# Kernel optimization log

Hardware: AMD Instinct MI355X
Metric: run time of the kernel (lower is better)

Reference implementation:

```python
import jax, jax.numpy as jnp
import numpy as np

IN_FEATURES = 4096
OUT_FEATURES = 4096
GROUP_SIZE = 128
TOKENS = 8192


def setup_inputs() -> dict:
    key = jax.random.key(0)
    k1, k2, k3 = jax.random.split(key, 3)
    x = jax.random.normal(k1, (TOKENS, IN_FEATURES), dtype=jnp.float32)
    weight_packed = jax.random.randint(k2, (OUT_FEATURES, IN_FEATURES // 2), 0, 256, dtype=jnp.int32)
    num_groups = IN_FEATURES // GROUP_SIZE
    weight_scales = jax.random.uniform(k3, (OUT_FEATURES, num_groups), dtype=jnp.float32) * 0.02
    return {"x": x, "weight_packed": weight_packed, "weight_scales": weight_scales, "group_size": GROUP_SIZE}


def _dequantize_int4(packed, scales, group_size):
    # packed: [N, K//2] int (uint8 values); scales: [N, G]
    out_features = packed.shape[0]
    in_features = packed.shape[1] * 2
    low = (packed & 15) - 8   # even columns
    high = ((packed >> 4) & 15) - 8  # odd columns
    # interleave low/high along last axis -> [N, K]
    unpacked = jnp.stack([low, high], axis=-1).reshape(out_features, in_features)
    num_groups = in_features // group_size
    w = unpacked.reshape(out_features, num_groups, group_size).astype(scales.dtype)
    w = w * scales[:, :, None]  # per-group scale
    return w.reshape(out_features, in_features)


def reference(x, weight_packed, weight_scales, group_size):
    W = _dequantize_int4(weight_packed, weight_scales, group_size)  # [N, K]
    # nn.functional.linear: x @ W.T (bias=False)
    return jnp.einsum('tk,nk->tn', x, W)
```

## Files before the change

### kernel.cpp

```cpp
#include <hip/hip_runtime.h>
#include <hip/hip_bf16.h>
#include <cstdint>
#include <cstddef>

#define TOKENS 8192
#define IN_F   4096
#define OUT_F  4096

typedef __bf16 bf16;
typedef bf16  bf16x8 __attribute__((ext_vector_type(8)));
typedef float f32x4  __attribute__((ext_vector_type(4)));

__global__ void prep_kernel(const float* __restrict__ xin, bf16* __restrict__ xout,
                            const int* __restrict__ wp, const float* __restrict__ sc,
                            bf16* __restrict__ wout) {
    if (blockIdx.x < 16384) {
        size_t i = ((size_t)blockIdx.x * 256 + threadIdx.x) * 8;
        const float4* p = (const float4*)(xin + i);
        float4 a = p[0], b = p[1];
        bf16x8 r;
        r[0] = (bf16)a.x; r[1] = (bf16)a.y; r[2] = (bf16)a.z; r[3] = (bf16)a.w;
        r[4] = (bf16)b.x; r[5] = (bf16)b.y; r[6] = (bf16)b.z; r[7] = (bf16)b.w;
        *(bf16x8*)(xout + i) = r;
    } else {
        int t  = (blockIdx.x - 16384) * 256 + threadIdx.x;
        int j0 = t << 2;
        int n  = j0 >> 11;
        int g  = (j0 & 2047) >> 6;
        float s = sc[(n << 5) + g];
        int4 p = *(const int4*)(wp + j0);
        bf16x8 r;
        r[0] = (bf16)((float)((p.x & 15) - 8) * s);
        r[1] = (bf16)((float)(((p.x >> 4) & 15) - 8) * s);
        r[2] = (bf16)((float)((p.y & 15) - 8) * s);
        r[3] = (bf16)((float)(((p.y >> 4) & 15) - 8) * s);
        r[4] = (bf16)((float)((p.z & 15) - 8) * s);
        r[5] = (bf16)((float)(((p.z >> 4) & 15) - 8) * s);
        r[6] = (bf16)((float)((p.w & 15) - 8) * s);
        r[7] = (bf16)((float)(((p.w >> 4) & 15) - 8) * s);
        *(bf16x8*)(wout + ((size_t)j0 << 1)) = r;
    }
}

__global__ void gemm_kernel(const bf16* __restrict__ A, const bf16* __restrict__ B,
                            float* __restrict__ C) {
    __shared__ char smem[32768] __attribute__((aligned(128)));

    const int tid  = threadIdx.x;
    const int lane = tid & 63;
    const int w    = tid >> 6;
    const int mt   = blockIdx.x >> 5;
    const int nt   = blockIdx.x & 31;

    const char* ga[4]; const char* gb[4]; int ldsoff[4];
#pragma unroll
    for (int t = 0; t < 4; ++t) {
        int c   = (w * 4 + t) * 64 + lane;
        int row = c >> 3;
        int g   = (c & 7) ^ (row & 7);
        ga[t] = (const char*)A + (size_t)(mt * 128 + row) * (IN_F * 2) + g * 16;
        gb[t] = (const char*)B + (size_t)(nt * 128 + row) * (IN_F * 2) + g * 16;
        ldsoff[t] = (w * 4 + t) * 1024;
    }

    const int m_lane = lane & 15;
    const int quad   = lane >> 4;
    const int sw     = m_lane & 7;
    const int m0     = (w >> 1) * 64;
    const int n0     = (w & 1) * 64;

    f32x4 acc[4][4];
#pragma unroll
    for (int i = 0; i < 4; ++i)
#pragma unroll
        for (int j = 0; j < 4; ++j) acc[i][j] = (f32x4)0.0f;

    const bf16x8* pA = (const bf16x8*)smem;
    const bf16x8* pB = (const bf16x8*)(smem + 16384);

    for (int kt = 0; kt < IN_F / 64; ++kt) {
#pragma unroll
        for (int t = 0; t < 4; ++t) {
            __builtin_amdgcn_global_load_lds(
                (const __attribute__((address_space(1))) void*)(ga[t] + kt * 128),
                (__attribute__((address_space(3))) void*)(smem + ldsoff[t]), 16, 0, 0);
            __builtin_amdgcn_global_load_lds(
                (const __attribute__((address_space(1))) void*)(gb[t] + kt * 128),
                (__attribute__((address_space(3))) void*)(smem + 16384 + ldsoff[t]), 16, 0, 0);
        }
        __syncthreads();

#pragma unroll
        for (int h = 0; h < 2; ++h) {
            const int slot = (h * 4 + quad) ^ sw;
            bf16x8 af[4], bfr[4];
#pragma unroll
            for (int i = 0; i < 4; ++i)
                af[i] = pA[(m0 + i * 16 + m_lane) * 8 + slot];
#pragma unroll
            for (int j = 0; j < 4; ++j)
                bfr[j] = pB[(n0 + j * 16 + m_lane) * 8 + slot];
#pragma unroll
            for (int i = 0; i < 4; ++i)
#pragma unroll
                for (int j = 0; j < 4; ++j)
                    acc[i][j] = __builtin_amdgcn_mfma_f32_16x16x32_bf16(af[i], bfr[j], acc[i][j], 0, 0, 0);
        }
        __syncthreads();
    }

    size_t crow0 = (size_t)(mt * 128 + m0 + quad * 4) * OUT_F + nt * 128 + n0 + m_lane;
#pragma unroll
    for (int i = 0; i < 4; ++i)
#pragma unroll
        for (int r = 0; r < 4; ++r) {
            float* cp = C + crow0 + (size_t)(i * 16 + r) * OUT_F;
#pragma unroll
            for (int j = 0; j < 4; ++j) cp[j * 16] = acc[i][j][r];
        }
}

__global__ void naive_kernel(const float* __restrict__ x, const int* __restrict__ wp,
                             const float* __restrict__ sc, float* __restrict__ out) {
    int o = blockIdx.x * 256 + threadIdx.x;
    int t = o >> 12, n = o & 4095;
    const float* xr = x + (size_t)t * IN_F;
    const int*   wr = wp + (size_t)n * (IN_F / 2);
    float acc = 0.f;
    for (int g = 0; g < 32; ++g) {
        float s = sc[n * 32 + g];
        float part = 0.f;
        for (int j = 0; j < 64; ++j) {
            int p = wr[g * 64 + j];
            part += xr[g * 128 + 2 * j]     * (float)((p & 15) - 8);
            part += xr[g * 128 + 2 * j + 1] * (float)(((p >> 4) & 15) - 8);
        }
        acc += part * s;
    }
    out[o] = acc;
}

extern "C" void kernel_launch(void* const* d_in, const int* in_sizes, int n_in,
                              void* d_out, int out_size, void* d_ws, size_t ws_size,
                              hipStream_t stream) {
    const float* x  = (const float*)d_in[0];
    const int*   wp = (const int*)d_in[1];
    const float* sc = (const float*)d_in[2];
    float* out = (float*)d_out;

    const size_t xb_bytes = (size_t)TOKENS * IN_F * 2;
    const size_t wb_bytes = (size_t)OUT_F * IN_F * 2;

    if (ws_size >= xb_bytes + wb_bytes) {
        bf16* xb = (bf16*)d_ws;
        bf16* wb = (bf16*)((char*)d_ws + xb_bytes);
        prep_kernel<<<dim3(16384 + 8192), dim3(256), 0, stream>>>(x, xb, wp, sc, wb);
        gemm_kernel<<<dim3((TOKENS / 128) * (OUT_F / 128)), dim3(256), 0, stream>>>(xb, wb, out);
    } else {
        naive_kernel<<<dim3((TOKENS * OUT_F) / 256), dim3(256), 0, stream>>>(x, wp, sc, out);
    }
}
```

Baseline: 483.2 us.

## Rewrite GEMM with 256x256 tiles, double-buffered LDS and interleaved load/MFMA schedule

The bf16 GEMM kernel moves from 128x128 tiles with 4 waves and a single LDS buffer to 256x256 tiles with 8 waves, a 128KB double-buffered LDS, and fine-grained interleaving of global-to-LDS loads with MFMA quarters under explicit barriers and vmcnt waits. It also remaps block indices so neighbouring workgroups share tiles for L2 reuse, and uses s_setprio around the MFMA blocks. The goal is to hide load latency and raise arithmetic intensity. In exchange it uses more registers and more LDS, which lowers occupancy, and the hand-written waitcnt schedule is fragile.

```diff
diff --git a/kernel.cpp b/kernel.cpp
--- a/kernel.cpp
+++ b/kernel.cpp
@@ -1,5 +1,4 @@
 #include <hip/hip_runtime.h>
-#include <hip/hip_bf16.h>
 #include <cstdint>
 #include <cstddef>
 
@@ -42,76 +41,126 @@
     }
 }
 
-__global__ void gemm_kernel(const bf16* __restrict__ A, const bf16* __restrict__ B,
-                            float* __restrict__ C) {
-    __shared__ char smem[32768] __attribute__((aligned(128)));
+
+#define GLL(src, dst) __builtin_amdgcn_global_load_lds( \
+    (const __attribute__((address_space(1))) void*)(src), \
+    (__attribute__((address_space(3))) void*)(dst), 16, 0, 0)
+#define BAR() asm volatile("s_barrier" ::: "memory")
+
+__global__ __launch_bounds__(512, 2)
+void gemm_kernel(const bf16* __restrict__ A, const bf16* __restrict__ B,
+                 float* __restrict__ C) {
+    __shared__ char smem[131072] __attribute__((aligned(128)));
 
     const int tid  = threadIdx.x;
     const int lane = tid & 63;
     const int w    = tid >> 6;
-    const int mt   = blockIdx.x >> 5;
-    const int nt   = blockIdx.x & 31;
-
-    const char* ga[4]; const char* gb[4]; int ldsoff[4];
-#pragma unroll
-    for (int t = 0; t < 4; ++t) {
-        int c   = (w * 4 + t) * 64 + lane;
-        int row = c >> 3;
-        int g   = (c & 7) ^ (row & 7);
-        ga[t] = (const char*)A + (size_t)(mt * 128 + row) * (IN_F * 2) + g * 16;
-        gb[t] = (const char*)B + (size_t)(nt * 128 + row) * (IN_F * 2) + g * 16;
-        ldsoff[t] = (w * 4 + t) * 1024;
-    }
-
-    const int m_lane = lane & 15;
-    const int quad   = lane >> 4;
-    const int sw     = m_lane & 7;
-    const int m0     = (w >> 1) * 64;
-    const int n0     = (w & 1) * 64;
-
-    f32x4 acc[4][4];
-#pragma unroll
-    for (int i = 0; i < 4; ++i)
+    const int wr   = w >> 2, wc = w & 3;
+    const int lrow = lane >> 3;
+    const int gsw  = (lane & 7) ^ lrow;
+
+    const int wg = ((blockIdx.x & 7) << 6) | (blockIdx.x >> 3);
+    const int mt = wg >> 4;
+    const int nt = wg & 15;
+
+    const char* Abase = (const char*)A + (size_t)(mt * 256) * (IN_F * 2);
+    const char* Bbase = (const char*)B + (size_t)(nt * 256) * (IN_F * 2);
+
+    const char* gA[4];
+#pragma unroll
+    for (int t = 0; t < 4; ++t)
+        gA[t] = Abase + (size_t)(t * 64 + w * 8 + lrow) * (IN_F * 2) + gsw * 16;
+    const int rb = (w >> 2) * 64 + (w & 3) * 8;
+    const int brow0 = rb, brow1 = rb + 128, brow2 = rb + 32, brow3 = rb + 160;
+    const char* gB[4];
+    gB[0] = Bbase + (size_t)(brow0 + lrow) * (IN_F * 2) + gsw * 16;
+    gB[1] = Bbase + (size_t)(brow1 + lrow) * (IN_F * 2) + gsw * 16;
+    gB[2] = Bbase + (size_t)(brow2 + lrow) * (IN_F * 2) + gsw * 16;
+    gB[3] = Bbase + (size_t)(brow3 + lrow) * (IN_F * 2) + gsw * 16;
+
+    char* const sm = smem;
+#define ST_A0(b, kt) { GLL(gA[0] + (kt) * 128, sm + (b) * 65536 +     0 + w * 1024); \
+                       GLL(gA[2] + (kt) * 128, sm + (b) * 65536 + 16384 + w * 1024); }
+#define ST_A1(b, kt) { GLL(gA[1] + (kt) * 128, sm + (b) * 65536 +  8192 + w * 1024); \
+                       GLL(gA[3] + (kt) * 128, sm + (b) * 65536 + 24576 + w * 1024); }
+#define ST_B0(b, kt) { GLL(gB[0] + (kt) * 128, sm + (b) * 65536 + 32768 + brow0 * 128); \
+                       GLL(gB[1] + (kt) * 128, sm + (b) * 65536 + 32768 + brow1 * 128); }
+#define ST_B1(b, kt) { GLL(gB[2] + (kt) * 128, sm + (b) * 65536 + 32768 + brow2 * 128); \
+                       GLL(gB[3] + (kt) * 128, sm + (b) * 65536 + 32768 + brow3 * 128); }
+
+    const int m_lane = lane & 15, quad = lane >> 4, sw = m_lane & 7;
+    const bf16x8* pA0 = (const bf16x8*)sm;
+    const bf16x8* pB0 = (const bf16x8*)(sm + 32768);
+    const bf16x8* pA1 = (const bf16x8*)(sm + 65536);
+    const bf16x8* pB1 = (const bf16x8*)(sm + 98304);
+
+    f32x4 acc[8][4];
+#pragma unroll
+    for (int i = 0; i < 8; ++i)
 #pragma unroll
         for (int j = 0; j < 4; ++j) acc[i][j] = (f32x4)0.0f;
 
-    const bf16x8* pA = (const bf16x8*)smem;
-    const bf16x8* pB = (const bf16x8*)(smem + 16384);
-
-    for (int kt = 0; kt < IN_F / 64; ++kt) {
-#pragma unroll
-        for (int t = 0; t < 4; ++t) {
-            __builtin_amdgcn_global_load_lds(
-                (const __attribute__((address_space(1))) void*)(ga[t] + kt * 128),
-                (__attribute__((address_space(3))) void*)(smem + ldsoff[t]), 16, 0, 0);
-            __builtin_amdgcn_global_load_lds(
-                (const __attribute__((address_space(1))) void*)(gb[t] + kt * 128),
-                (__attribute__((address_space(3))) void*)(smem + 16384 + ldsoff[t]), 16, 0, 0);
-        }
-        __syncthreads();
-
-#pragma unroll
-        for (int h = 0; h < 2; ++h) {
-            const int slot = (h * 4 + quad) ^ sw;
-            bf16x8 af[4], bfr[4];
-#pragma unroll
-            for (int i = 0; i < 4; ++i)
-                af[i] = pA[(m0 + i * 16 + m_lane) * 8 + slot];
-#pragma unroll
-            for (int j = 0; j < 4; ++j)
-                bfr[j] = pB[(n0 + j * 16 + m_lane) * 8 + slot];
-#pragma unroll
-            for (int i = 0; i < 4; ++i)
-#pragma unroll
-                for (int j = 0; j < 4; ++j)
-                    acc[i][j] = __builtin_amdgcn_mfma_f32_16x16x32_bf16(af[i], bfr[j], acc[i][j], 0, 0, 0);
-        }
-        __syncthreads();
-    }
-
-    size_t crow0 = (size_t)(mt * 128 + m0 + quad * 4) * OUT_F + nt * 128 + n0 + m_lane;
-#pragma unroll
-    for (int i = 0; i < 4; ++i)
+    ST_A0(0, 0); ST_B0(0, 0); ST_B1(0, 0); ST_A1(0, 0);
+    ST_A0(1, 1); ST_B0(1, 1); ST_B1(1, 1);
+    asm volatile("s_waitcnt vmcnt(6)" ::: "memory");
+    BAR();
+
+#define LDA(PA, qr) \
+    { _Pragma("unroll") for (int i = 0; i < 4; ++i) { \
+        _Pragma("unroll") for (int kh = 0; kh < 2; ++kh) { \
+            af[i][kh] = (PA)[(wr * 128 + ((qr) * 4 + i) * 16 + m_lane) * 8 + ((kh * 4 + quad) ^ sw)]; } } }
+#define LDB(PB) \
+    { _Pragma("unroll") for (int j = 0; j < 4; ++j) { \
+        _Pragma("unroll") for (int kh = 0; kh < 2; ++kh) { \
+            bfr[j][kh] = (PB)[(wc * 64 + j * 16 + m_lane) * 8 + ((kh * 4 + quad) ^ sw)]; } } }
+#define MM(qr, qc) \
+    { __builtin_amdgcn_s_setprio(1); \
+      _Pragma("unroll") for (int i = 0; i < 4; ++i) { \
+        _Pragma("unroll") for (int j = 0; j < 2; ++j) { \
+          _Pragma("unroll") for (int kh = 0; kh < 2; ++kh) { \
+            acc[(qr) * 4 + i][(qc) * 2 + j] = __builtin_amdgcn_mfma_f32_16x16x32_bf16( \
+                af[i][kh], bfr[(qc) * 2 + j][kh], acc[(qr) * 4 + i][(qc) * 2 + j], 0, 0, 0); } } } \
+      __builtin_amdgcn_s_setprio(0); }
+
+    for (int it = 0; it < 32; ++it) {
+        const int kt0 = 2 * it;
+        const int kt1 = kt0 + 1;
+        const bool more = (it < 31);
+        {
+            bf16x8 af[4][2], bfr[4][2];
+            LDA(pA0, 0); LDB(pB0);
+            ST_A1(1, kt1);
+            BAR(); MM(0, 0); BAR();
+            if (more) ST_A0(0, kt0 + 2);
+            BAR(); MM(0, 1); BAR();
+            LDA(pA0, 1);
+            if (more) ST_B0(0, kt0 + 2);
+            BAR(); MM(1, 0); BAR();
+            if (more) ST_B1(0, kt0 + 2);
+            if (more) { asm volatile("s_waitcnt vmcnt(6)" ::: "memory"); }
+            else      { asm volatile("s_waitcnt vmcnt(0)" ::: "memory"); }
+            BAR(); MM(1, 1); BAR();
+        }
+        {
+            bf16x8 af[4][2], bfr[4][2];
+            LDA(pA1, 0); LDB(pB1);
+            if (more) ST_A1(0, kt1 + 1);
+            BAR(); MM(0, 0); BAR();
+            if (more) ST_A0(1, kt1 + 2);
+            BAR(); MM(0, 1); BAR();
+            LDA(pA1, 1);
+            if (more) ST_B0(1, kt1 + 2);
+            BAR(); MM(1, 0); BAR();
+            if (more) ST_B1(1, kt1 + 2);
+            if (more) { asm volatile("s_waitcnt vmcnt(6)" ::: "memory"); }
+            BAR(); MM(1, 1); BAR();
+        }
+    }
+
+    const size_t crow0 = (size_t)(mt * 256 + wr * 128 + quad * 4) * OUT_F
+                       + (size_t)(nt * 256 + wc * 64 + m_lane);
+#pragma unroll
+    for (int i = 0; i < 8; ++i)
 #pragma unroll
         for (int r = 0; r < 4; ++r) {
             float* cp = C + crow0 + (size_t)(i * 16 + r) * OUT_F;
@@ -125,13 +174,13 @@
     int o = blockIdx.x * 256 + threadIdx.x;
     int t = o >> 12, n = o & 4095;
     const float* xr = x + (size_t)t * IN_F;
-    const int*   wr = wp + (size_t)n * (IN_F / 2);
+    const int*   wr2 = wp + (size_t)n * (IN_F / 2);
     float acc = 0.f;
     for (int g = 0; g < 32; ++g) {
         float s = sc[n * 32 + g];
         float part = 0.f;
         for (int j = 0; j < 64; ++j) {
-            int p = wr[g * 64 + j];
+            int p = wr2[g * 64 + j];
             part += xr[g * 128 + 2 * j]     * (float)((p & 15) - 8);
             part += xr[g * 128 + 2 * j + 1] * (float)(((p >> 4) & 15) - 8);
         }
@@ -155,7 +204,7 @@
         bf16* xb = (bf16*)d_ws;
         bf16* wb = (bf16*)((char*)d_ws + xb_bytes);
         prep_kernel<<<dim3(16384 + 8192), dim3(256), 0, stream>>>(x, xb, wp, sc, wb);
-        gemm_kernel<<<dim3((TOKENS / 128) * (OUT_F / 128)), dim3(256), 0, stream>>>(xb, wb, out);
+        gemm_kernel<<<dim3((TOKENS / 256) * (OUT_F / 256)), dim3(512), 0, stream>>>(xb, wb, out);
     } else {
         naive_kernel<<<dim3((TOKENS * OUT_F) / 256), dim3(256), 0, stream>>>(x, wp, sc, out);
     }
```

Result: no change. 473.9 us (-1.9%).
